# Kernel tuning notes

Hardware: AMD Instinct MI355X
Metric: run time of the kernel (lower is better)

The kernel has to match this reference:

```python
import jax, jax.numpy as jnp
import numpy as np

B, H, W, EMB = 8, 128, 128, 6
NF = 256  # number_of_filters


def setup_inputs() -> dict:
    key = jax.random.key(0)
    ks = jax.random.split(key, 12)
    s = 0.02  # init_func-style small normal init
    image = jax.random.normal(ks[0], (B, 1, H, W), jnp.float32)
    mask_embedding = jax.random.normal(ks[1], (B, EMB, H, W), jnp.float32)
    # conv stack: 134->256 (s2), 256->512 (s2), 512->1024 (s2), 1024->1024 (s2), avgpool8, 1024->128 (1x1)
    w0 = jax.random.normal(ks[2], (NF, W + EMB, 4, 4), jnp.float32) * s
    b0 = jnp.zeros((NF,), jnp.float32)
    w1 = jax.random.normal(ks[3], (2 * NF, NF, 4, 4), jnp.float32) * s
    b1 = jnp.zeros((2 * NF,), jnp.float32)
    w2 = jax.random.normal(ks[4], (4 * NF, 2 * NF, 4, 4), jnp.float32) * s
    b2 = jnp.zeros((4 * NF,), jnp.float32)
    w3 = jax.random.normal(ks[5], (4 * NF, 4 * NF, 4, 4), jnp.float32) * s
    b3 = jnp.zeros((4 * NF,), jnp.float32)
    w4 = jax.random.normal(ks[6], (W, 4 * NF, 1, 1), jnp.float32) * s
    b4 = jnp.zeros((W,), jnp.float32)
    return dict(image=image, mask_embedding=mask_embedding,
                w0=w0, b0=b0, w1=w1, b1=b1, w2=w2, b2=b2, w3=w3, b3=b3, w4=w4, b4=b4)


def _spectral_map(image, mask_embedding):
    # Original: kspace = fft2(image); for each column i zero out all other k-space
    # columns, ifft2 (unnormalized torch.ifft => 1/(H*W)), take real part.
    # Since only column i is nonzero, ifft2 separates:
    #   sep[b,i,h,w] = Re( (1/W) * ifft_H(kspace[:, :, i])[h] * exp(2j*pi*w*i/W) )
    Bv, _, Hv, Wv = image.shape
    kspace = jnp.fft.fft2(image[:, 0])                    # (B, H, W) complex64
    col = jnp.fft.ifft(kspace, axis=1) / Wv               # (B, H, W_i); ifft over height gives 1/H
    idx = jnp.arange(Wv)
    twiddle = jnp.exp((2j * jnp.pi / Wv) * jnp.outer(idx, idx).astype(jnp.float32))  # (W_spatial, W_i) complex64
    sep = jnp.real(jnp.einsum('bhi,wi->bihw', col, twiddle))  # (B, W, H, W) float32
    return jnp.concatenate([sep, mask_embedding], axis=1)     # (B, W+EMB, H, W)


def _conv(x, w, b, stride):
    y = jax.lax.conv_general_dilated(x, w, (stride, stride), [(1, 1), (1, 1)],
                                     dimension_numbers=('NCHW', 'OIHW', 'NCHW'))
    return y + b[None, :, None, None]


def _inorm(x):  # InstanceNorm2d, affine=False, eps=1e-5
    m = jnp.mean(x, (2, 3), keepdims=True)
    v = jnp.var(x, (2, 3), keepdims=True)
    return (x - m) * jax.lax.rsqrt(v + 1e-5)


def _lrelu(x):
    return jax.nn.leaky_relu(x, 0.2)


def reference(image, mask_embedding, w0, b0, w1, b1, w2, b2, w3, b3, w4, b4):
    x = _spectral_map(image, mask_embedding)       # (B, 134, 128, 128)
    x = _lrelu(_conv(x, w0, b0, 2))                # (B, 256, 64, 64)
    x = _lrelu(_inorm(_conv(x, w1, b1, 2)))        # (B, 512, 32, 32)
    x = _lrelu(_inorm(_conv(x, w2, b2, 2)))        # (B, 1024, 16, 16)
    x = _lrelu(_inorm(_conv(x, w3, b3, 2)))        # (B, 1024, 8, 8)
    pooled = jnp.mean(x, (2, 3))                   # AvgPool(k=8) -> (B, 1024)
    out = jnp.einsum('bc,oc->bo', pooled, w4[:, :, 0, 0]) + b4  # 1x1 conv + squeeze -> (B, 128)
    return out
```

## Files before the change

kernel.cpp:

```cpp
#include <hip/hip_runtime.h>
#include <hip/hip_bf16.h>
#include <cstdint>
#include <cstddef>

typedef __attribute__((ext_vector_type(8))) short bf16x8;
typedef __attribute__((ext_vector_type(4))) float f32x4;

#define PI2F 6.283185307179586f

__device__ __forceinline__ float bf2f(unsigned short u) {
  union { float f; uint32_t i; } x; x.i = ((uint32_t)u) << 16; return x.f;
}
__device__ __forceinline__ unsigned short f2bf(float f) {
  union { float f; uint32_t i; } x; x.f = f;
  uint32_t r = x.i + 0x7FFF + ((x.i >> 16) & 1);
  return (unsigned short)(r >> 16);
}

__device__ __forceinline__ void glds16(const void* g, void* l) {
  __builtin_amdgcn_global_load_lds(
      (const __attribute__((address_space(1))) unsigned int*)g,
      (__attribute__((address_space(3))) unsigned int*)l, 16, 0, 0);
}

__global__ void zinit_kernel(unsigned short* __restrict__ zp, unsigned short* __restrict__ pad) {
  int t = threadIdx.x;
  zp[t] = 0;
  pad[t] = 0;
}

__global__ void dft_kernel(const float* __restrict__ img, float2* __restrict__ col,
                           float2* __restrict__ tw) {
  __shared__ float row[128];
  __shared__ float2 twl[128];
  const int bh = blockIdx.x;
  const int i = threadIdx.x;
  row[i] = img[bh * 128 + i];
  float s, c;
  sincosf(PI2F * (float)i / 128.0f, &s, &c);
  twl[i] = make_float2(c, s);
  __syncthreads();
  if (bh == 0) tw[i] = twl[i];
  float sr = 0.f, si = 0.f;
  for (int w = 0; w < 128; ++w) {
    float v = row[w];
    float2 t = twl[(i * w) & 127];
    sr += v * t.x;
    si -= v * t.y;
  }
  col[bh * 128 + i] = make_float2(sr * (1.0f / 128.0f), si * (1.0f / 128.0f));
}

__global__ __launch_bounds__(256)
void sep_cl2_kernel(const float2* __restrict__ col, const float2* __restrict__ tw,
                    const float* __restrict__ maskE, unsigned short* __restrict__ x0) {
  __shared__ float2 cl[128];
  __shared__ float2 twl[128];
  const int bh = blockIdx.x;
  const int b = bh >> 7, h = bh & 127;
  const int tid = threadIdx.x;
  if (tid < 128) {
    cl[tid] = col[(b * 128 + h) * 128 + tid];
    twl[tid] = tw[tid];
  }
  __syncthreads();
  const int p = tid >> 1;
  const int c0 = (tid & 1) * 64;
  unsigned short* dst = x0 + ((size_t)bh * 128 + p) * 144;
#pragma unroll
  for (int j = 0; j < 16; ++j) {
    ushort4 o;
#pragma unroll
    for (int q = 0; q < 4; ++q) {
      int c = c0 + 4 * j + q;
      float2 cv = cl[c];
      float2 t = twl[(p * c) & 127];
      float v = cv.x * t.x - cv.y * t.y;
      ((unsigned short*)&o)[q] = f2bf(v);
    }
    *reinterpret_cast<ushort4*>(dst + c0 + 4 * j) = o;
  }
  if (tid < 128) {
    const int w = tid;
    float v[6];
#pragma unroll
    for (int cm = 0; cm < 6; ++cm)
      v[cm] = maskE[(((size_t)(b * 6 + cm) * 128) + h) * 128 + w];
    unsigned short* d2 = x0 + ((size_t)bh * 128 + w) * 144 + 128;
    ushort4 m0, m1, mz;
    m0.x = f2bf(v[0]); m0.y = f2bf(v[1]); m0.z = f2bf(v[2]); m0.w = f2bf(v[3]);
    m1.x = f2bf(v[4]); m1.y = f2bf(v[5]); m1.z = 0; m1.w = 0;
    mz.x = 0; mz.y = 0; mz.z = 0; mz.w = 0;
    reinterpret_cast<ushort4*>(d2)[0] = m0;
    reinterpret_cast<ushort4*>(d2)[1] = m1;
    reinterpret_cast<ushort4*>(d2)[2] = mz;
    reinterpret_cast<ushort4*>(d2)[3] = mz;
  }
}

template<int CIN, int CINP>
__global__ __launch_bounds__(256)
void cvtperm_kernel(const float* __restrict__ src, unsigned short* __restrict__ dst) {
  __shared__ unsigned short tile[16][68];
  const int m = blockIdx.y;
  const int ci0 = blockIdx.x * 64;
  const int tid = threadIdx.x;
  {
    const int ci = ci0 + (tid >> 2);
    const int t0 = (tid & 3) * 4;
    float4 v = make_float4(0.f, 0.f, 0.f, 0.f);
    if (ci < CIN) v = *reinterpret_cast<const float4*>(&src[((size_t)m * CIN + ci) * 16 + t0]);
    const int cr = tid >> 2;
    tile[t0 + 0][cr] = f2bf(v.x);
    tile[t0 + 1][cr] = f2bf(v.y);
    tile[t0 + 2][cr] = f2bf(v.z);
    tile[t0 + 3][cr] = f2bf(v.w);
  }
  __syncthreads();
  {
    const int t = tid >> 4;
    const int co = (tid & 15) * 4;
    const int ci = ci0 + co;
    if (ci < CINP) {
      ushort4 o;
      o.x = tile[t][co]; o.y = tile[t][co + 1]; o.z = tile[t][co + 2]; o.w = tile[t][co + 3];
      *reinterpret_cast<ushort4*>(&dst[(size_t)m * (16 * CINP) + (size_t)t * CINP + ci]) = o;
    }
  }
}

template<int CINP, int CSTOR, int COUT, int HI, int WI, int HO, int WO, int NSPLIT, bool FUSED>
__global__ __launch_bounds__(256, 2)
void conv_cl5_kernel(const unsigned short* __restrict__ X,
                     const unsigned short* __restrict__ Wt,
                     const unsigned short* __restrict__ zp,
                     const float* __restrict__ bias,
                     unsigned short* __restrict__ Y,
                     float* __restrict__ P) {
  constexpr int KTOT = 16 * CINP;
  constexpr int CPT = CINP / 32;
  constexpr int HOWO = HO * WO;
  constexpr int LHW = __builtin_ctz(HOWO);
  constexpr int LWO = __builtin_ctz(WO);
  constexpr int TPS = 16 / NSPLIT;
  constexpr size_t PSTRIDE = (size_t)8 * HOWO * COUT;
  constexpr int NIT = TPS * CPT;

  __shared__ __align__(16) unsigned short As[4][4096];
  __shared__ __align__(16) unsigned short Bs[4][4096];

  const int tid = threadIdx.x;
  const int lane = tid & 63;
  const int wv = tid >> 6;
  const int wm = wv >> 1, wn = wv & 1;
  const int n0 = blockIdx.x * 128;
  const int m0 = blockIdx.y * 128;
  const int split = blockIdx.z;
  const int r = lane & 15, g = lane >> 4;

  const int row0 = tid >> 2;
  const int row1 = row0 + 64;
  const int chk = tid & 3;
  const int kofs = (((chk - ((row0 >> 1) & 3)) & 3)) * 8;

  int bb0, bho0, bwo0, bb1, bho1, bwo1;
  {
    int rn0 = n0 + row0, rn1 = n0 + row1;
    bb0 = rn0 >> LHW; bb1 = rn1 >> LHW;
    int re0 = rn0 & (HOWO - 1), re1 = rn1 & (HOWO - 1);
    bho0 = re0 >> LWO; bho1 = re1 >> LWO;
    bwo0 = re0 & (WO - 1); bwo1 = re1 & (WO - 1);
  }

  const int tap0 = split * TPS;
  int tapI = tap0, ccI = 0;
  size_t boff0, boff1; bool bok0, bok1;
  auto tap_geom = [&](int t) {
    int kh = t >> 2, kw = t & 3;
    {
      int h = 2 * bho0 - 1 + kh, w = 2 * bwo0 - 1 + kw;
      bool hv = (unsigned)h < (unsigned)HI, wvv = (unsigned)w < (unsigned)WI;
      bok0 = hv && wvv;
      boff0 = (((size_t)bb0 * HI + (hv ? h : 0)) * WI + (wvv ? w : 0)) * (size_t)CSTOR;
    }
    {
      int h = 2 * bho1 - 1 + kh, w = 2 * bwo1 - 1 + kw;
      bool hv = (unsigned)h < (unsigned)HI, wvv = (unsigned)w < (unsigned)WI;
      bok1 = hv && wvv;
      boff1 = (((size_t)bb1 * HI + (hv ? h : 0)) * WI + (wvv ? w : 0)) * (size_t)CSTOR;
    }
  };
  tap_geom(tapI);

  auto issue = [&](int buf) {
    const int kk = tapI * CINP + ccI * 32 + kofs;
    glds16(Wt + (size_t)(m0 + row0) * KTOT + kk, &As[buf][wv * 512]);
    glds16(Wt + (size_t)(m0 + row1) * KTOT + kk, &As[buf][2048 + wv * 512]);
    const int ci = ccI * 32 + kofs;
    glds16(bok0 ? (X + boff0 + ci) : zp, &Bs[buf][wv * 512]);
    glds16(bok1 ? (X + boff1 + ci) : zp, &Bs[buf][2048 + wv * 512]);
  };
  auto advance = [&]() {
    ccI++;
    if (ccI == CPT) { ccI = 0; tapI++; if (tapI < tap0 + TPS) tap_geom(tapI); }
  };

  f32x4 acc[4][4] = {};

  issue(0); advance();
  issue(1); advance();
  issue(2); advance();

  for (int it = 0; it < NIT; ++it) {
    if (it + 2 < NIT)      asm volatile("s_waitcnt vmcnt(8)" ::: "memory");
    else if (it + 1 < NIT) asm volatile("s_waitcnt vmcnt(4)" ::: "memory");
    else                   asm volatile("s_waitcnt vmcnt(0)" ::: "memory");
    __builtin_amdgcn_s_barrier();
    __builtin_amdgcn_sched_barrier(0);
    if (it + 3 < NIT) { issue((it + 3) & 3); advance(); }
    const int buf = it & 3;
    bf16x8 af[4], bf[4];
#pragma unroll
    for (int mi = 0; mi < 4; ++mi) {
      int rw = wm * 64 + mi * 16 + r;
      af[mi] = *reinterpret_cast<const bf16x8*>(
          &As[buf][rw * 32 + (((g + ((rw >> 1) & 3)) & 3) * 8)]);
    }
#pragma unroll
    for (int ni = 0; ni < 4; ++ni) {
      int rw = wn * 64 + ni * 16 + r;
      bf[ni] = *reinterpret_cast<const bf16x8*>(
          &Bs[buf][rw * 32 + (((g + ((rw >> 1) & 3)) & 3) * 8)]);
    }
#pragma unroll
    for (int mi = 0; mi < 4; ++mi)
#pragma unroll
      for (int ni = 0; ni < 4; ++ni)
        acc[mi][ni] = __builtin_amdgcn_mfma_f32_16x16x32_bf16(af[mi], bf[ni], acc[mi][ni], 0, 0, 0);
  }

#pragma unroll
  for (int ni = 0; ni < 4; ++ni) {
    int n = n0 + wn * 64 + ni * 16 + r;
    int b = n >> LHW;
    int rem = n & (HOWO - 1);
    size_t obase = ((size_t)b * HOWO + rem) * COUT;
#pragma unroll
    for (int mi = 0; mi < 4; ++mi) {
      int mb = m0 + wm * 64 + mi * 16 + g * 4;
      f32x4 a = acc[mi][ni];
      if constexpr (FUSED) {
        float v0 = a[0] + bias[mb + 0]; v0 = v0 > 0.f ? v0 : 0.2f * v0;
        float v1 = a[1] + bias[mb + 1]; v1 = v1 > 0.f ? v1 : 0.2f * v1;
        float v2 = a[2] + bias[mb + 2]; v2 = v2 > 0.f ? v2 : 0.2f * v2;
        float v3 = a[3] + bias[mb + 3]; v3 = v3 > 0.f ? v3 : 0.2f * v3;
        ushort4 o;
        o.x = f2bf(v0); o.y = f2bf(v1); o.z = f2bf(v2); o.w = f2bf(v3);
        *reinterpret_cast<ushort4*>(&Y[obase + mb]) = o;
      } else {
        *reinterpret_cast<float4*>(&P[split * PSTRIDE + obase + mb]) =
            make_float4(a[0], a[1], a[2], a[3]);
      }
    }
  }
}

template<int HOWO, int COUT, int NSPLIT>
__global__ __launch_bounds__(256)
void inorm_cl3_kernel(const float* __restrict__ P, unsigned short* __restrict__ Y) {
  constexpr int PER = HOWO / 32;
  constexpr size_t PSTRIDE = (size_t)8 * HOWO * COUT;
  const int b = blockIdx.y;
  const int cl = threadIdx.x & 7;
  const int c = blockIdx.x * 8 + cl;
  const int hw0 = threadIdx.x >> 3;
  const float* base = P + ((size_t)b * HOWO) * COUT + c;
  float v[PER];
  float s1 = 0.f, s2 = 0.f;
#pragma unroll
  for (int j = 0; j < PER; ++j) {
    int hw = hw0 + j * 32;
    float x = 0.f;
#pragma unroll
    for (int s = 0; s < NSPLIT; ++s) x += base[s * PSTRIDE + (size_t)hw * COUT];
    v[j] = x; s1 += x; s2 += x * x;
  }
  __shared__ float r1[32][9], r2[32][9];
  __shared__ float ms[8], rs[8];
  r1[hw0][cl] = s1; r2[hw0][cl] = s2;
  __syncthreads();
  if (threadIdx.x < 8) {
    float a1 = 0.f, a2 = 0.f;
#pragma unroll
    for (int i = 0; i < 32; ++i) { a1 += r1[i][threadIdx.x]; a2 += r2[i][threadIdx.x]; }
    float mean = a1 * (1.0f / HOWO);
    float var = a2 * (1.0f / HOWO) - mean * mean;
    ms[threadIdx.x] = mean;
    rs[threadIdx.x] = rsqrtf(var + 1e-5f);
  }
  __syncthreads();
  const float mean = ms[cl], rstd = rs[cl];
  unsigned short* yb = Y + ((size_t)b * HOWO) * COUT + c;
#pragma unroll
  for (int j = 0; j < PER; ++j) {
    int hw = hw0 + j * 32;
    float t = (v[j] - mean) * rstd;
    t = t > 0.f ? t : 0.2f * t;
    yb[(size_t)hw * COUT] = f2bf(t);
  }
}

__global__ __launch_bounds__(256)
void pool_cl_kernel(const unsigned short* __restrict__ X, float* __restrict__ pooled) {
  const int b = blockIdx.x;
  const int c4 = threadIdx.x * 4;
  float4 acc = make_float4(0.f, 0.f, 0.f, 0.f);
  for (int hw = 0; hw < 64; ++hw) {
    ushort4 v = *reinterpret_cast<const ushort4*>(&X[((size_t)b * 64 + hw) * 1024 + c4]);
    acc.x += bf2f(v.x); acc.y += bf2f(v.y); acc.z += bf2f(v.z); acc.w += bf2f(v.w);
  }
  acc.x *= (1.0f / 64.0f); acc.y *= (1.0f / 64.0f);
  acc.z *= (1.0f / 64.0f); acc.w *= (1.0f / 64.0f);
  *reinterpret_cast<float4*>(&pooled[b * 1024 + c4]) = acc;
}

__global__ __launch_bounds__(64)
void fc_kernel(const float* __restrict__ pooled, const float* __restrict__ w4,
               const float* __restrict__ b4, float* __restrict__ out) {
  const int bo = blockIdx.x;
  const int b = bo >> 7, o = bo & 127;
  const int lane = threadIdx.x;
  float s = 0.f;
#pragma unroll
  for (int j = 0; j < 16; ++j) {
    int c = lane + j * 64;
    s += pooled[b * 1024 + c] * w4[o * 1024 + c];
  }
#pragma unroll
  for (int off = 32; off > 0; off >>= 1) s += __shfl_xor(s, off);
  if (lane == 0) out[bo] = s + b4[o];
}

extern "C" void kernel_launch(void* const* d_in, const int* in_sizes, int n_in,
                              void* d_out, int out_size, void* d_ws, size_t ws_size,
                              hipStream_t stream) {
  (void)in_sizes; (void)n_in; (void)out_size; (void)ws_size;
  const float* image = (const float*)d_in[0];
  const float* maskE = (const float*)d_in[1];
  const float* w0 = (const float*)d_in[2];
  const float* b0 = (const float*)d_in[3];
  const float* w1 = (const float*)d_in[4];
  const float* w2 = (const float*)d_in[6];
  const float* w3 = (const float*)d_in[8];
  const float* w4 = (const float*)d_in[10];
  const float* b4 = (const float*)d_in[11];
  float* out = (float*)d_out;

  char* ws = (char*)d_ws;
  size_t off = 0;
  auto alloc = [&](size_t bytes) -> void* {
    void* p = ws + off;
    off = (off + bytes + 255) & ~(size_t)255;
    return p;
  };

  const size_t X0BYTES = (size_t)8 * 128 * 128 * 144 * 2;
  unsigned short* wbuf = (unsigned short*)alloc((size_t)1024 * 16384 * 2);
  char* bufA = (char*)alloc(X0BYTES + 256);
  char* bufB = (char*)alloc((size_t)8 * 4096 * 256 * 2);
  float2* col = (float2*)alloc((size_t)131072 * sizeof(float2));
  float2* tw = (float2*)alloc(128 * sizeof(float2));
  float* pooled = (float*)alloc(8192 * 4);
  unsigned short* zp = (unsigned short*)alloc(256);

  unsigned short* x0 = (unsigned short*)bufA;
  unsigned short* x0pad = (unsigned short*)(bufA + X0BYTES);
  float* part = (float*)bufA;
  unsigned short* a0 = (unsigned short*)bufB;
  unsigned short* a1 = (unsigned short*)bufB;
  unsigned short* a2 = (unsigned short*)bufB;
  unsigned short* a3 = (unsigned short*)bufB;

  zinit_kernel<<<1, 128, 0, stream>>>(zp, x0pad);

  dft_kernel<<<1024, 128, 0, stream>>>(image, col, tw);
  sep_cl2_kernel<<<1024, 256, 0, stream>>>(col, tw, maskE, x0);

  cvtperm_kernel<134, 160><<<dim3(3, 256), 256, 0, stream>>>(w0, wbuf);
  conv_cl5_kernel<160, 144, 256, 128, 128, 64, 64, 1, true>
      <<<dim3(256, 2, 1), 256, 0, stream>>>(x0, wbuf, zp, b0, a0, nullptr);

  cvtperm_kernel<256, 256><<<dim3(4, 512), 256, 0, stream>>>(w1, wbuf);
  conv_cl5_kernel<256, 256, 512, 64, 64, 32, 32, 2, false>
      <<<dim3(64, 4, 2), 256, 0, stream>>>(a0, wbuf, zp, nullptr, nullptr, part);
  inorm_cl3_kernel<1024, 512, 2><<<dim3(64, 8), 256, 0, stream>>>(part, a1);

  cvtperm_kernel<512, 512><<<dim3(8, 1024), 256, 0, stream>>>(w2, wbuf);
  conv_cl5_kernel<512, 512, 1024, 32, 32, 16, 16, 4, false>
      <<<dim3(16, 8, 4), 256, 0, stream>>>(a1, wbuf, zp, nullptr, nullptr, part);
  inorm_cl3_kernel<256, 1024, 4><<<dim3(128, 8), 256, 0, stream>>>(part, a2);

  cvtperm_kernel<1024, 1024><<<dim3(16, 1024), 256, 0, stream>>>(w3, wbuf);
  conv_cl5_kernel<1024, 1024, 1024, 16, 16, 8, 8, 16, false>
      <<<dim3(4, 8, 16), 256, 0, stream>>>(a2, wbuf, zp, nullptr, nullptr, part);
  inorm_cl3_kernel<64, 1024, 16><<<dim3(128, 8), 256, 0, stream>>>(part, a3);

  pool_cl_kernel<<<8, 256, 0, stream>>>(a3, pooled);
  fc_kernel<<<1024, 64, 0, stream>>>(pooled, w4, b4, out);
}
```

Baseline: 338.0 us.

## Shrink conv GEMM tile to 128x64 with two waves and triple buffering

The implicit-GEMM conv kernel now uses 128-thread blocks (2 waves) computing 128x64 output tiles instead of 256-thread 128x128 tiles. Each wave owns 64 output channels across all 64 pixels. The LDS pipeline drops from four to three stages with smaller B buffers, and MFMA sections are wrapped in s_setprio. The aim is more blocks and less LDS per block, giving better occupancy and wave-level overlap, at the cost of less reuse of the weight tile per loaded activation.

Measured after the change: 368.7 us. +9.1%, slower.

```diff
diff --git a/kernel.cpp b/kernel.cpp
--- a/kernel.cpp
+++ b/kernel.cpp
@@ -130,8 +130,8 @@
 }
 
 template<int CINP, int CSTOR, int COUT, int HI, int WI, int HO, int WO, int NSPLIT, bool FUSED>
-__global__ __launch_bounds__(256, 2)
-void conv_cl5_kernel(const unsigned short* __restrict__ X,
+__global__ __launch_bounds__(128, 2)
+void conv_cl6_kernel(const unsigned short* __restrict__ X,
                      const unsigned short* __restrict__ Wt,
                      const unsigned short* __restrict__ zp,
                      const float* __restrict__ bias,
@@ -146,26 +146,25 @@
   constexpr size_t PSTRIDE = (size_t)8 * HOWO * COUT;
   constexpr int NIT = TPS * CPT;
 
-  __shared__ __align__(16) unsigned short As[4][4096];
-  __shared__ __align__(16) unsigned short Bs[4][4096];
+  __shared__ __align__(16) unsigned short As[3][4096];
+  __shared__ __align__(16) unsigned short Bs[3][2048];
 
   const int tid = threadIdx.x;
   const int lane = tid & 63;
   const int wv = tid >> 6;
-  const int wm = wv >> 1, wn = wv & 1;
-  const int n0 = blockIdx.x * 128;
+  const int n0 = blockIdx.x * 64;
   const int m0 = blockIdx.y * 128;
   const int split = blockIdx.z;
   const int r = lane & 15, g = lane >> 4;
-
-  const int row0 = tid >> 2;
-  const int row1 = row0 + 64;
+  const int slot = (((g + ((r >> 1) & 3)) & 3)) * 8;
+
+  const int sr = tid >> 2;
   const int chk = tid & 3;
-  const int kofs = (((chk - ((row0 >> 1) & 3)) & 3)) * 8;
+  const int kofs = (((chk - ((sr >> 1) & 3)) & 3)) * 8;
 
   int bb0, bho0, bwo0, bb1, bho1, bwo1;
   {
-    int rn0 = n0 + row0, rn1 = n0 + row1;
+    int rn0 = n0 + sr, rn1 = n0 + sr + 32;
     bb0 = rn0 >> LHW; bb1 = rn1 >> LHW;
     int re0 = rn0 & (HOWO - 1), re1 = rn1 & (HOWO - 1);
     bho0 = re0 >> LWO; bho1 = re1 >> LWO;
@@ -194,11 +193,14 @@
 
   auto issue = [&](int buf) {
     const int kk = tapI * CINP + ccI * 32 + kofs;
-    glds16(Wt + (size_t)(m0 + row0) * KTOT + kk, &As[buf][wv * 512]);
-    glds16(Wt + (size_t)(m0 + row1) * KTOT + kk, &As[buf][2048 + wv * 512]);
+    const unsigned short* wb = Wt + (size_t)(m0 + sr) * KTOT + kk;
+    glds16(wb,                       &As[buf][(wv * 16) * 32]);
+    glds16(wb + (size_t)32 * KTOT,   &As[buf][(32 + wv * 16) * 32]);
+    glds16(wb + (size_t)64 * KTOT,   &As[buf][(64 + wv * 16) * 32]);
+    glds16(wb + (size_t)96 * KTOT,   &As[buf][(96 + wv * 16) * 32]);
     const int ci = ccI * 32 + kofs;
-    glds16(bok0 ? (X + boff0 + ci) : zp, &Bs[buf][wv * 512]);
-    glds16(bok1 ? (X + boff1 + ci) : zp, &Bs[buf][2048 + wv * 512]);
+    glds16(bok0 ? (X + boff0 + ci) : zp, &Bs[buf][(wv * 16) * 32]);
+    glds16(bok1 ? (X + boff1 + ci) : zp, &Bs[buf][(32 + wv * 16) * 32]);
   };
   auto advance = [&]() {
     ccI++;
@@ -209,45 +211,41 @@
 
   issue(0); advance();
   issue(1); advance();
-  issue(2); advance();
-
+
+  int buf = 0, nbuf = 2;
   for (int it = 0; it < NIT; ++it) {
-    if (it + 2 < NIT)      asm volatile("s_waitcnt vmcnt(8)" ::: "memory");
-    else if (it + 1 < NIT) asm volatile("s_waitcnt vmcnt(4)" ::: "memory");
-    else                   asm volatile("s_waitcnt vmcnt(0)" ::: "memory");
+    if (it + 1 < NIT) asm volatile("s_waitcnt vmcnt(6)" ::: "memory");
+    else              asm volatile("s_waitcnt vmcnt(0)" ::: "memory");
     __builtin_amdgcn_s_barrier();
     __builtin_amdgcn_sched_barrier(0);
-    if (it + 3 < NIT) { issue((it + 3) & 3); advance(); }
-    const int buf = it & 3;
+    if (it + 2 < NIT) { issue(nbuf); advance(); }
     bf16x8 af[4], bf[4];
 #pragma unroll
-    for (int mi = 0; mi < 4; ++mi) {
-      int rw = wm * 64 + mi * 16 + r;
-      af[mi] = *reinterpret_cast<const bf16x8*>(
-          &As[buf][rw * 32 + (((g + ((rw >> 1) & 3)) & 3) * 8)]);
-    }
-#pragma unroll
-    for (int ni = 0; ni < 4; ++ni) {
-      int rw = wn * 64 + ni * 16 + r;
-      bf[ni] = *reinterpret_cast<const bf16x8*>(
-          &Bs[buf][rw * 32 + (((g + ((rw >> 1) & 3)) & 3) * 8)]);
-    }
+    for (int mi = 0; mi < 4; ++mi)
+      af[mi] = *reinterpret_cast<const bf16x8*>(&As[buf][(wv * 64 + mi * 16 + r) * 32 + slot]);
+#pragma unroll
+    for (int ni = 0; ni < 4; ++ni)
+      bf[ni] = *reinterpret_cast<const bf16x8*>(&Bs[buf][(ni * 16 + r) * 32 + slot]);
+    __builtin_amdgcn_s_setprio(1);
 #pragma unroll
     for (int mi = 0; mi < 4; ++mi)
 #pragma unroll
       for (int ni = 0; ni < 4; ++ni)
         acc[mi][ni] = __builtin_amdgcn_mfma_f32_16x16x32_bf16(af[mi], bf[ni], acc[mi][ni], 0, 0, 0);
+    __builtin_amdgcn_s_setprio(0);
+    buf = buf == 2 ? 0 : buf + 1;
+    nbuf = nbuf == 2 ? 0 : nbuf + 1;
   }
 
 #pragma unroll
   for (int ni = 0; ni < 4; ++ni) {
-    int n = n0 + wn * 64 + ni * 16 + r;
+    int n = n0 + ni * 16 + r;
     int b = n >> LHW;
     int rem = n & (HOWO - 1);
     size_t obase = ((size_t)b * HOWO + rem) * COUT;
 #pragma unroll
     for (int mi = 0; mi < 4; ++mi) {
-      int mb = m0 + wm * 64 + mi * 16 + g * 4;
+      int mb = m0 + wv * 64 + mi * 16 + g * 4;
       f32x4 a = acc[mi][ni];
       if constexpr (FUSED) {
         float v0 = a[0] + bias[mb + 0]; v0 = v0 > 0.f ? v0 : 0.2f * v0;
@@ -387,22 +385,22 @@
   sep_cl2_kernel<<<1024, 256, 0, stream>>>(col, tw, maskE, x0);
 
   cvtperm_kernel<134, 160><<<dim3(3, 256), 256, 0, stream>>>(w0, wbuf);
-  conv_cl5_kernel<160, 144, 256, 128, 128, 64, 64, 1, true>
-      <<<dim3(256, 2, 1), 256, 0, stream>>>(x0, wbuf, zp, b0, a0, nullptr);
+  conv_cl6_kernel<160, 144, 256, 128, 128, 64, 64, 1, true>
+      <<<dim3(512, 2, 1), 128, 0, stream>>>(x0, wbuf, zp, b0, a0, nullptr);
 
   cvtperm_kernel<256, 256><<<dim3(4, 512), 256, 0, stream>>>(w1, wbuf);
-  conv_cl5_kernel<256, 256, 512, 64, 64, 32, 32, 2, false>
-      <<<dim3(64, 4, 2), 256, 0, stream>>>(a0, wbuf, zp, nullptr, nullptr, part);
+  conv_cl6_kernel<256, 256, 512, 64, 64, 32, 32, 2, false>
+      <<<dim3(128, 4, 2), 128, 0, stream>>>(a0, wbuf, zp, nullptr, nullptr, part);
   inorm_cl3_kernel<1024, 512, 2><<<dim3(64, 8), 256, 0, stream>>>(part, a1);
 
   cvtperm_kernel<512, 512><<<dim3(8, 1024), 256, 0, stream>>>(w2, wbuf);
-  conv_cl5_kernel<512, 512, 1024, 32, 32, 16, 16, 4, false>
-      <<<dim3(16, 8, 4), 256, 0, stream>>>(a1, wbuf, zp, nullptr, nullptr, part);
+  conv_cl6_kernel<512, 512, 1024, 32, 32, 16, 16, 4, false>
+      <<<dim3(32, 8, 4), 128, 0, stream>>>(a1, wbuf, zp, nullptr, nullptr, part);
   inorm_cl3_kernel<256, 1024, 4><<<dim3(128, 8), 256, 0, stream>>>(part, a2);
 
   cvtperm_kernel<1024, 1024><<<dim3(16, 1024), 256, 0, stream>>>(w3, wbuf);
-  conv_cl5_kernel<1024, 1024, 1024, 16, 16, 8, 8, 16, false>
-      <<<dim3(4, 8, 16), 256, 0, stream>>>(a2, wbuf, zp, nullptr, nullptr, part);
+  conv_cl6_kernel<1024, 1024, 1024, 16, 16, 8, 8, 16, false>
+      <<<dim3(8, 8, 16), 128, 0, stream>>>(a2, wbuf, zp, nullptr, nullptr, part);
   inorm_cl3_kernel<64, 1024, 16><<<dim3(128, 8), 256, 0, stream>>>(part, a3);
 
   pool_cl_kernel<<<8, 256, 0, stream>>>(a3, pooled);
```
